# Kernel optimization log

Hardware: AMD Instinct MI355X
Metric: run time of the kernel (lower is better)

Reference implementation:

```python
import jax, jax.numpy as jnp
import numpy as np

N_USERS = 100000
N_ITEMS = 50000
N_NODES = N_USERS + N_ITEMS
EMB = 64
N_LAYERS = 3
N_EDGES = 4800000
AVG_DEG = 32


def setup_inputs() -> dict:
    key = jax.random.key(0)
    k1, k2, k3, k4, k5 = jax.random.split(key, 5)
    user_emb = jax.random.normal(k1, (N_USERS, EMB), dtype=jnp.float32) * 0.01
    item_emb = jax.random.normal(k2, (N_ITEMS, EMB), dtype=jnp.float32) * 0.01
    # normalized adjacency values ~ 1/deg
    adj_val = jax.random.uniform(k3, (N_EDGES,), dtype=jnp.float32) * (1.0 / AVG_DEG)
    adj_row = jax.random.randint(k4, (N_EDGES,), 0, N_NODES, dtype=jnp.int32)
    adj_col = jax.random.randint(k5, (N_EDGES,), 0, N_NODES, dtype=jnp.int32)
    return {"user_emb": user_emb, "item_emb": item_emb,
            "adj_val": adj_val, "adj_row": adj_row, "adj_col": adj_col}


def reference(user_emb, item_emb, adj_val, adj_row, adj_col):
    ego = jnp.concatenate([user_emb, item_emb], axis=0)  # [N_NODES, EMB]

    def spmm(x):
        # sparse_adj @ x via gather + segment-sum over destination rows
        msgs = adj_val[:, None] * x[adj_col]              # [N_EDGES, EMB]
        return jax.ops.segment_sum(msgs, adj_row, num_segments=N_NODES)

    acc = ego  # running sum for layer-mean (avoids stacking all layers)
    x = ego
    for _ in range(N_LAYERS):
        x = jax.nn.relu(spmm(x))
        acc = acc + x
    all_emb = acc / (N_LAYERS + 1)
    return all_emb[:N_USERS], all_emb[N_USERS:]
```

## Files before the change

kernel.cpp:

```cpp
#include <hip/hip_runtime.h>

#define N_USERS 100000
#define N_ITEMS 50000
#define N_NODES 150000
#define EMB 64
#define N_EDGES 4800000
#define N_LAYERS 3

#define RPB 128
#define NB 1172
#define CAP 4608
#define CHUNK 8192
#define EPT (CHUNK / 512)
#define NCHUNKS ((N_EDGES + CHUNK - 1) / CHUNK)
#define LS_EPT (CAP / 256)

__global__ __launch_bounds__(256) void init_kernel(
        const float2* __restrict__ user, const float2* __restrict__ item,
        unsigned short* __restrict__ x8, float* __restrict__ xs,
        float2* __restrict__ out) {
    int t = threadIdx.x;
    int p = t & 31;
    int r = blockIdx.x * 8 + (t >> 5);
    if (r >= N_NODES) return;
    float2 e = (r < N_USERS) ? user[r * 32 + p] : item[(r - N_USERS) * 32 + p];
    int o = r * 32 + p;
    out[o] = make_float2(0.25f * e.x, 0.25f * e.y);
    float m = fmaxf(fabsf(e.x), fabsf(e.y));
    #pragma unroll
    for (int mask = 16; mask; mask >>= 1) m = fmaxf(m, __shfl_xor(m, mask));
    float inv = (m > 0.f) ? 127.0f / m : 0.f;
    int q0 = (int)rintf(e.x * inv) + 128;
    int q1 = (int)rintf(e.y * inv) + 128;
    x8[o] = (unsigned short)(q0 | (q1 << 8));
    if (p == 0) xs[r] = m * (1.0f / 127.0f);
}

__global__ __launch_bounds__(512) void chunkscatter_kernel(
        const int* __restrict__ row, const int* __restrict__ col,
        const float* __restrict__ val,
        int* __restrict__ cursor, int2* __restrict__ sEdge) {
    __shared__ int2 rec[CHUNK];
    __shared__ unsigned short bidS[CHUNK];
    __shared__ int cnt[NB];
    __shared__ int lofs[NB];
    __shared__ int gbase[NB];
    __shared__ int tmp[512];

    int t = threadIdx.x;
    int e0 = blockIdx.x * CHUNK;
    int n = N_EDGES - e0; if (n > CHUNK) n = CHUNK;

    for (int i = t; i < NB; i += 512) cnt[i] = 0;
    __syncthreads();

    int2 myrec[EPT];
    int  myb[EPT];
    #pragma unroll
    for (int j = 0; j < EPT; ++j) {
        int i = j * 512 + t;
        if (i < n) {
            int gi = e0 + i;
            int r = row[gi];
            int b = r >> 7;
            myrec[j] = make_int2(((r & (RPB - 1)) << 18) | col[gi],
                                 __float_as_int(val[gi]));
            myb[j] = b;
            atomicAdd(&cnt[b], 1);
        } else myb[j] = -1;
    }
    __syncthreads();

    int b3 = t * 3;
    int c0 = (b3     < NB) ? cnt[b3]     : 0;
    int c1 = (b3 + 1 < NB) ? cnt[b3 + 1] : 0;
    int c2 = (b3 + 2 < NB) ? cnt[b3 + 2] : 0;
    int s = c0 + c1 + c2;
    tmp[t] = s;
    __syncthreads();
    for (int off = 1; off < 512; off <<= 1) {
        int u = (t >= off) ? tmp[t - off] : 0;
        __syncthreads();
        tmp[t] += u;
        __syncthreads();
    }
    int excl = tmp[t] - s;
    if (b3     < NB) lofs[b3]     = excl;
    if (b3 + 1 < NB) lofs[b3 + 1] = excl + c0;
    if (b3 + 2 < NB) lofs[b3 + 2] = excl + c0 + c1;
    __syncthreads();

    for (int i = t; i < NB; i += 512) {
        int c = cnt[i];
        gbase[i] = c ? atomicAdd(&cursor[i], c) : 0;
        cnt[i] = lofs[i];
    }
    __syncthreads();

    #pragma unroll
    for (int j = 0; j < EPT; ++j) {
        if (myb[j] >= 0) {
            int p = atomicAdd(&cnt[myb[j]], 1);
            rec[p] = myrec[j];
            bidS[p] = (unsigned short)myb[j];
        }
    }
    __syncthreads();

    for (int i = t; i < n; i += 512) {
        int b = bidS[i];
        int pos = gbase[b] + (i - lofs[b]);
        if (pos < CAP) sEdge[b * CAP + pos] = rec[i];
    }
}

__global__ __launch_bounds__(256, 4) void localsort_kernel(
        const int* __restrict__ cursor, int2* __restrict__ sEdge,
        int* __restrict__ rowStart, int* __restrict__ rowCnt) {
    __shared__ int lh[RPB];
    __shared__ int lsc[RPB];
    __shared__ int lcur[RPB];
    int b = blockIdx.x, t = threadIdx.x;
    int s0 = b * CAP;
    int size = cursor[b]; if (size > CAP) size = CAP;

    int2 e[LS_EPT];
    #pragma unroll
    for (int j = 0; j < LS_EPT; ++j) {
        int idx = j * 256 + t;
        if (idx < size) e[j] = sEdge[s0 + idx];
    }
    if (t < RPB) lh[t] = 0;
    __syncthreads();
    #pragma unroll
    for (int j = 0; j < LS_EPT; ++j) {
        if (j * 256 + t < size) atomicAdd(&lh[e[j].x >> 18], 1);
    }
    __syncthreads();
    if (t < RPB) lsc[t] = lh[t];
    __syncthreads();
    for (int off = 1; off < RPB; off <<= 1) {
        int u = 0;
        if (t < RPB && t >= off) u = lsc[t - off];
        __syncthreads();
        if (t < RPB) lsc[t] += u;
        __syncthreads();
    }
    if (t < RPB) {
        int excl = lsc[t] - lh[t];
        lcur[t] = excl;
        int node = b * RPB + t;
        if (node < N_NODES) {
            rowStart[node] = s0 + excl;
            rowCnt[node]   = lh[t];
        }
    }
    __syncthreads();
    #pragma unroll
    for (int j = 0; j < LS_EPT; ++j) {
        if (j * 256 + t < size) {
            int rl = e[j].x >> 18;
            int pos = atomicAdd(&lcur[rl], 1);
            sEdge[s0 + pos] = make_int2((e[j].x & 0x3FFFF) << 6, e[j].y);
        }
    }
}

template<int BIASED>
__global__ __launch_bounds__(256, 4) void gather_kernel(
        const int* __restrict__ rowStart, const int* __restrict__ rowCnt,
        const int2* __restrict__ sEdge,
        const unsigned short* __restrict__ x8, const float* __restrict__ xs,
        unsigned short* __restrict__ y8, float* __restrict__ ys,
        float2* __restrict__ out, int last) {
    __shared__ int2 eds[8][32];
    int t = threadIdx.x;
    int p = t & 31;
    int h = t >> 5;
    int r = blockIdx.x * 8 + h;
    if (r >= N_NODES) return;
    int start = rowStart[r];
    int end   = start + rowCnt[r];
    float2 acc = make_float2(0.f, 0.f);
    float ws = 0.f;
    const char* __restrict__ xp = (const char*)x8 + 2 * p;

    for (int base = start; base < end; base += 32) {
        int idx = base + p;
        int2 ed = (idx < end) ? sEdge[idx] : make_int2(0, 0);
        float w0 = __int_as_float(ed.y) * xs[ed.x >> 6];
        eds[h][p] = make_int2(ed.x, __float_as_int(w0));

        int cnt = end - base; if (cnt > 32) cnt = 32;
        int nb = (cnt + 7) >> 3;
        for (int s8 = 0; s8 < nb; ++s8) {
            #pragma unroll
            for (int jj = 0; jj < 8; ++jj) {
                int2 e = eds[h][s8 * 8 + jj];
                float w = __int_as_float(e.y);
                unsigned q = *(const unsigned short*)(xp + e.x);
                acc.x = fmaf(w, (float)(q & 0xFFu), acc.x);
                acc.y = fmaf(w, (float)((q >> 8) & 0xFFu), acc.y);
                if (BIASED) ws += w;
            }
        }
    }
    if (BIASED) {
        acc.x = fmaf(-128.f, ws, acc.x);
        acc.y = fmaf(-128.f, ws, acc.y);
    }

    float rx = fmaxf(acc.x, 0.f);
    float ry = fmaxf(acc.y, 0.f);
    int o = r * 32 + p;
    float2 ov = out[o];
    ov.x += 0.25f * rx; ov.y += 0.25f * ry;
    out[o] = ov;
    if (!last) {
        float m = fmaxf(rx, ry);
        #pragma unroll
        for (int mask = 16; mask; mask >>= 1) m = fmaxf(m, __shfl_xor(m, mask));
        float inv = (m > 0.f) ? 255.0f / m : 0.f;
        int q0 = (int)(rx * inv + 0.5f);
        int q1 = (int)(ry * inv + 0.5f);
        y8[o] = (unsigned short)(q0 | (q1 << 8));
        if (p == 0) ys[r] = m * (1.0f / 255.0f);
    }
}

extern "C" void kernel_launch(void* const* d_in, const int* in_sizes, int n_in,
                              void* d_out, int out_size, void* d_ws, size_t ws_size,
                              hipStream_t stream) {
    const float* user_emb = (const float*)d_in[0];
    const float* item_emb = (const float*)d_in[1];
    const float* adj_val  = (const float*)d_in[2];
    const int*   adj_row  = (const int*)d_in[3];
    const int*   adj_col  = (const int*)d_in[4];
    float* out = (float*)d_out;

    char* p = (char*)d_ws;
    int*  cursor   = (int*)p;  p += ((size_t)NB * 4 + 15) & ~15ull;
    int*  rowStart = (int*)p;  p += ((size_t)N_NODES * 4 + 15) & ~15ull;
    int*  rowCnt   = (int*)p;  p += ((size_t)N_NODES * 4 + 15) & ~15ull;
    int2* sEdge    = (int2*)p; p += (size_t)NB * CAP * 8;
    unsigned short* xq0 = (unsigned short*)p; p += (size_t)N_NODES * EMB;
    unsigned short* xq1 = (unsigned short*)p; p += (size_t)N_NODES * EMB;
    float* xsc0    = (float*)p; p += (size_t)N_NODES * 4;
    float* xsc1    = (float*)p;

    hipMemsetAsync(cursor, 0, (size_t)NB * 4, stream);

    init_kernel<<<(N_NODES + 7) / 8, 256, 0, stream>>>(
        (const float2*)user_emb, (const float2*)item_emb,
        xq0, xsc0, (float2*)out);

    chunkscatter_kernel<<<NCHUNKS, 512, 0, stream>>>(
        adj_row, adj_col, adj_val, cursor, sEdge);

    localsort_kernel<<<NB, 256, 0, stream>>>(cursor, sEdge, rowStart, rowCnt);

    const int rowBlocks = (N_NODES + 7) / 8;
    unsigned short* x = xq0; float* sx = xsc0;
    unsigned short* y = xq1; float* sy = xsc1;
    for (int l = 0; l < N_LAYERS; ++l) {
        if (l == 0)
            gather_kernel<1><<<rowBlocks, 256, 0, stream>>>(
                rowStart, rowCnt, sEdge, x, sx, y, sy, (float2*)out, 0);
        else
            gather_kernel<0><<<rowBlocks, 256, 0, stream>>>(
                rowStart, rowCnt, sEdge, x, sx, y, sy, (float2*)out, l == N_LAYERS - 1);
        unsigned short* tq = x; x = y; y = tq;
        float* ts = sx; sx = sy; sy = ts;
    }
}
```

Before: 538.9 us.

## Sort edges by column group and sweep groups across persistent row tiles

The local sort now bins each row's edges into five source-column ranges and records per-row group offsets. The gather kernel becomes a persistent-style sweep where each warp owns 20 rows, keeps 20 accumulators in registers, and walks all rows' edges one column group at a time. The aim is to keep the gathered source embeddings for the current column range resident in cache so that random gathers hit L2/MALL more often. In exchange it raises register pressure, uses a fixed 960-block grid that may balance load poorly, and serialises rows within a warp, which reduces parallelism.

```diff
diff --git a/kernel.cpp b/kernel.cpp
--- a/kernel.cpp
+++ b/kernel.cpp
@@ -14,6 +14,11 @@
 #define EPT (CHUNK / 512)
 #define NCHUNKS ((N_EDGES + CHUNK - 1) / CHUNK)
 #define LS_EPT (CAP / 256)
+
+#define GRP 5
+#define BINS (RPB * GRP)
+#define GRID 960
+#define TPB_T 20
 
 __global__ __launch_bounds__(256) void init_kernel(
         const float2* __restrict__ user, const float2* __restrict__ item,
@@ -116,10 +121,11 @@
 
 __global__ __launch_bounds__(256, 4) void localsort_kernel(
         const int* __restrict__ cursor, int2* __restrict__ sEdge,
-        int* __restrict__ rowStart, int* __restrict__ rowCnt) {
-    __shared__ int lh[RPB];
-    __shared__ int lsc[RPB];
-    __shared__ int lcur[RPB];
+        int* __restrict__ grpStart) {
+    __shared__ int lh[BINS];
+    __shared__ int lofs[BINS];
+    __shared__ int lcur[BINS];
+    __shared__ int tmp[256];
     int b = blockIdx.x, t = threadIdx.x;
     int s0 = b * CAP;
     int size = cursor[b]; if (size > CAP) size = CAP;
@@ -130,101 +136,132 @@
         int idx = j * 256 + t;
         if (idx < size) e[j] = sEdge[s0 + idx];
     }
-    if (t < RPB) lh[t] = 0;
-    __syncthreads();
-    #pragma unroll
-    for (int j = 0; j < LS_EPT; ++j) {
-        if (j * 256 + t < size) atomicAdd(&lh[e[j].x >> 18], 1);
-    }
-    __syncthreads();
-    if (t < RPB) lsc[t] = lh[t];
-    __syncthreads();
-    for (int off = 1; off < RPB; off <<= 1) {
-        int u = 0;
-        if (t < RPB && t >= off) u = lsc[t - off];
-        __syncthreads();
-        if (t < RPB) lsc[t] += u;
-        __syncthreads();
-    }
-    if (t < RPB) {
-        int excl = lsc[t] - lh[t];
-        lcur[t] = excl;
-        int node = b * RPB + t;
-        if (node < N_NODES) {
-            rowStart[node] = s0 + excl;
-            rowCnt[node]   = lh[t];
-        }
-    }
+    for (int i = t; i < BINS; i += 256) lh[i] = 0;
     __syncthreads();
     #pragma unroll
     for (int j = 0; j < LS_EPT; ++j) {
         if (j * 256 + t < size) {
             int rl = e[j].x >> 18;
-            int pos = atomicAdd(&lcur[rl], 1);
+            int g  = (e[j].x & 0x3FFFF) >> 15;
+            atomicAdd(&lh[rl * GRP + g], 1);
+        }
+    }
+    __syncthreads();
+    int b3 = t * 3;
+    int c0 = (b3     < BINS) ? lh[b3]     : 0;
+    int c1 = (b3 + 1 < BINS) ? lh[b3 + 1] : 0;
+    int c2 = (b3 + 2 < BINS) ? lh[b3 + 2] : 0;
+    int s = c0 + c1 + c2;
+    tmp[t] = s;
+    __syncthreads();
+    for (int off = 1; off < 256; off <<= 1) {
+        int u = (t >= off) ? tmp[t - off] : 0;
+        __syncthreads();
+        tmp[t] += u;
+        __syncthreads();
+    }
+    int excl = tmp[t] - s;
+    if (b3     < BINS) { lofs[b3]     = excl;           lcur[b3]     = excl; }
+    if (b3 + 1 < BINS) { lofs[b3 + 1] = excl + c0;      lcur[b3 + 1] = excl + c0; }
+    if (b3 + 2 < BINS) { lofs[b3 + 2] = excl + c0 + c1; lcur[b3 + 2] = excl + c0 + c1; }
+    __syncthreads();
+    if (t < RPB) {
+        int node = b * RPB + t;
+        if (node < N_NODES) {
+            #pragma unroll
+            for (int g = 0; g < GRP; ++g)
+                grpStart[node * 6 + g] = s0 + lofs[t * GRP + g];
+            int endbin = t * GRP + GRP;
+            grpStart[node * 6 + 5] = s0 + ((endbin < BINS) ? lofs[endbin] : size);
+        }
+    }
+    __syncthreads();
+    #pragma unroll
+    for (int j = 0; j < LS_EPT; ++j) {
+        if (j * 256 + t < size) {
+            int rl = e[j].x >> 18;
+            int g  = (e[j].x & 0x3FFFF) >> 15;
+            int pos = atomicAdd(&lcur[rl * GRP + g], 1);
             sEdge[s0 + pos] = make_int2((e[j].x & 0x3FFFF) << 6, e[j].y);
         }
     }
 }
 
-template<int BIASED>
-__global__ __launch_bounds__(256, 4) void gather_kernel(
-        const int* __restrict__ rowStart, const int* __restrict__ rowCnt,
-        const int2* __restrict__ sEdge,
+template<int BIASED, int LAST>
+__global__ __launch_bounds__(256, 4) void gather_sweep(
+        const int* __restrict__ grpStart, const int2* __restrict__ sEdge,
         const unsigned short* __restrict__ x8, const float* __restrict__ xs,
         unsigned short* __restrict__ y8, float* __restrict__ ys,
-        float2* __restrict__ out, int last) {
+        float2* __restrict__ out) {
     __shared__ int2 eds[8][32];
     int t = threadIdx.x;
     int p = t & 31;
     int h = t >> 5;
-    int r = blockIdx.x * 8 + h;
-    if (r >= N_NODES) return;
-    int start = rowStart[r];
-    int end   = start + rowCnt[r];
-    float2 acc = make_float2(0.f, 0.f);
-    float ws = 0.f;
-    const char* __restrict__ xp = (const char*)x8 + 2 * p;
-
-    for (int base = start; base < end; base += 32) {
-        int idx = base + p;
-        int2 ed = (idx < end) ? sEdge[idx] : make_int2(0, 0);
-        float w0 = __int_as_float(ed.y) * xs[ed.x >> 6];
-        eds[h][p] = make_int2(ed.x, __float_as_int(w0));
-
-        int cnt = end - base; if (cnt > 32) cnt = 32;
-        int nb = (cnt + 7) >> 3;
-        for (int s8 = 0; s8 < nb; ++s8) {
-            #pragma unroll
-            for (int jj = 0; jj < 8; ++jj) {
-                int2 e = eds[h][s8 * 8 + jj];
-                float w = __int_as_float(e.y);
-                unsigned q = *(const unsigned short*)(xp + e.x);
-                acc.x = fmaf(w, (float)(q & 0xFFu), acc.x);
-                acc.y = fmaf(w, (float)((q >> 8) & 0xFFu), acc.y);
-                if (BIASED) ws += w;
+    int rbase = blockIdx.x * (TPB_T * 8) + h;
+    const char* xp = (const char*)x8 + 2 * p;
+
+    float2 acc[TPB_T];
+    float  ws[BIASED ? TPB_T : 1];
+    #pragma unroll
+    for (int j = 0; j < TPB_T; ++j) acc[j] = make_float2(0.f, 0.f);
+    if (BIASED) {
+        #pragma unroll
+        for (int j = 0; j < TPB_T; ++j) ws[j] = 0.f;
+    }
+
+    for (int g = 0; g < GRP; ++g) {
+        #pragma unroll
+        for (int j = 0; j < TPB_T; ++j) {
+            int r = rbase + j * 8;
+            if (r < N_NODES) {
+                int st = grpStart[r * 6 + g];
+                int en = grpStart[r * 6 + g + 1];
+                for (int base = st; base < en; base += 32) {
+                    int idx = base + p;
+                    int2 ed = (idx < en) ? sEdge[idx] : make_int2(0, 0);
+                    float w0 = __int_as_float(ed.y) * xs[ed.x >> 6];
+                    eds[h][p] = make_int2(ed.x, __float_as_int(w0));
+                    int cnt = en - base; if (cnt > 32) cnt = 32;
+                    int nb = (cnt + 7) >> 3;
+                    for (int s8 = 0; s8 < nb; ++s8) {
+                        #pragma unroll
+                        for (int jj = 0; jj < 8; ++jj) {
+                            int2 ee = eds[h][s8 * 8 + jj];
+                            float w = __int_as_float(ee.y);
+                            unsigned q = *(const unsigned short*)(xp + ee.x);
+                            acc[j].x = fmaf(w, (float)(q & 0xFFu), acc[j].x);
+                            acc[j].y = fmaf(w, (float)((q >> 8) & 0xFFu), acc[j].y);
+                            if (BIASED) ws[j] += w;
+                        }
+                    }
+                }
             }
         }
     }
-    if (BIASED) {
-        acc.x = fmaf(-128.f, ws, acc.x);
-        acc.y = fmaf(-128.f, ws, acc.y);
-    }
-
-    float rx = fmaxf(acc.x, 0.f);
-    float ry = fmaxf(acc.y, 0.f);
-    int o = r * 32 + p;
-    float2 ov = out[o];
-    ov.x += 0.25f * rx; ov.y += 0.25f * ry;
-    out[o] = ov;
-    if (!last) {
-        float m = fmaxf(rx, ry);
-        #pragma unroll
-        for (int mask = 16; mask; mask >>= 1) m = fmaxf(m, __shfl_xor(m, mask));
-        float inv = (m > 0.f) ? 255.0f / m : 0.f;
-        int q0 = (int)(rx * inv + 0.5f);
-        int q1 = (int)(ry * inv + 0.5f);
-        y8[o] = (unsigned short)(q0 | (q1 << 8));
-        if (p == 0) ys[r] = m * (1.0f / 255.0f);
+
+    #pragma unroll
+    for (int j = 0; j < TPB_T; ++j) {
+        int r = rbase + j * 8;
+        if (r < N_NODES) {
+            float ax = acc[j].x, ay = acc[j].y;
+            if (BIASED) { ax = fmaf(-128.f, ws[j], ax); ay = fmaf(-128.f, ws[j], ay); }
+            float rx = fmaxf(ax, 0.f);
+            float ry = fmaxf(ay, 0.f);
+            int o = r * 32 + p;
+            float2 ov = out[o];
+            ov.x += 0.25f * rx; ov.y += 0.25f * ry;
+            out[o] = ov;
+            if (!LAST) {
+                float m = fmaxf(rx, ry);
+                #pragma unroll
+                for (int mask = 16; mask; mask >>= 1) m = fmaxf(m, __shfl_xor(m, mask));
+                float inv = (m > 0.f) ? 255.0f / m : 0.f;
+                int q0 = (int)(rx * inv + 0.5f);
+                int q1 = (int)(ry * inv + 0.5f);
+                y8[o] = (unsigned short)(q0 | (q1 << 8));
+                if (p == 0) ys[r] = m * (1.0f / 255.0f);
+            }
+        }
     }
 }
 
@@ -240,8 +277,7 @@
 
     char* p = (char*)d_ws;
     int*  cursor   = (int*)p;  p += ((size_t)NB * 4 + 15) & ~15ull;
-    int*  rowStart = (int*)p;  p += ((size_t)N_NODES * 4 + 15) & ~15ull;
-    int*  rowCnt   = (int*)p;  p += ((size_t)N_NODES * 4 + 15) & ~15ull;
+    int*  grpStart = (int*)p;  p += ((size_t)N_NODES * 6 * 4 + 15) & ~15ull;
     int2* sEdge    = (int2*)p; p += (size_t)NB * CAP * 8;
     unsigned short* xq0 = (unsigned short*)p; p += (size_t)N_NODES * EMB;
     unsigned short* xq1 = (unsigned short*)p; p += (size_t)N_NODES * EMB;
@@ -257,19 +293,12 @@
     chunkscatter_kernel<<<NCHUNKS, 512, 0, stream>>>(
         adj_row, adj_col, adj_val, cursor, sEdge);
 
-    localsort_kernel<<<NB, 256, 0, stream>>>(cursor, sEdge, rowStart, rowCnt);
-
-    const int rowBlocks = (N_NODES + 7) / 8;
-    unsigned short* x = xq0; float* sx = xsc0;
-    unsigned short* y = xq1; float* sy = xsc1;
-    for (int l = 0; l < N_LAYERS; ++l) {
-        if (l == 0)
-            gather_kernel<1><<<rowBlocks, 256, 0, stream>>>(
-                rowStart, rowCnt, sEdge, x, sx, y, sy, (float2*)out, 0);
-        else
-            gather_kernel<0><<<rowBlocks, 256, 0, stream>>>(
-                rowStart, rowCnt, sEdge, x, sx, y, sy, (float2*)out, l == N_LAYERS - 1);
-        unsigned short* tq = x; x = y; y = tq;
-        float* ts = sx; sx = sy; sy = ts;
-    }
-}
+    localsort_kernel<<<NB, 256, 0, stream>>>(cursor, sEdge, grpStart);
+
+    gather_sweep<1, 0><<<GRID, 256, 0, stream>>>(
+        grpStart, sEdge, xq0, xsc0, xq1, xsc1, (float2*)out);
+    gather_sweep<0, 0><<<GRID, 256, 0, stream>>>(
+        grpStart, sEdge, xq1, xsc1, xq0, xsc0, (float2*)out);
+    gather_sweep<0, 1><<<GRID, 256, 0, stream>>>(
+        grpStart, sEdge, xq0, xsc0, xq1, xsc1, (float2*)out);
+}
```

Measured after the change: 725.6 us. +34.6%, slower.
